# Kernel optimization log

Measured on AMD Instinct MI355X. Metric: run time of the kernel, lower is better.

Reference implementation:

```python
import jax, jax.numpy as jnp
import numpy as np

L, B, H, P = 2048, 16, 512, 256
EPS = 1e-6  # flax nnx LayerNorm default


def setup_inputs() -> dict:
    key = jax.random.key(0)
    ks = jax.random.split(key, 12)
    x = jax.random.normal(ks[0], (L, B, H), jnp.float32)
    d = jax.random.bernoulli(ks[1], 0.01, (L, B))  # sparse reset signal
    hidden_re = jnp.zeros((1, B, P), jnp.float32)
    hidden_im = jnp.zeros((1, B, P), jnp.float32)
    # S5 diagonal state matrix (stable: Re < 0)
    Lambda_re = -0.5 * jnp.exp(0.5 * jax.random.normal(ks[2], (P,), jnp.float32))
    Lambda_im = np.float32(np.pi) * jax.random.normal(ks[3], (P,), jnp.float32)
    B_re = jax.random.normal(ks[4], (P, H), jnp.float32) / np.sqrt(2.0 * H).astype(np.float32)
    B_im = jax.random.normal(ks[5], (P, H), jnp.float32) / np.sqrt(2.0 * H).astype(np.float32)
    C_re = jax.random.normal(ks[6], (H, P), jnp.float32) / np.sqrt(P).astype(np.float32)
    C_im = jax.random.normal(ks[7], (H, P), jnp.float32) / np.sqrt(P).astype(np.float32)
    D = jax.random.normal(ks[8], (H,), jnp.float32)
    log_step = jax.random.uniform(ks[9], (P,), jnp.float32,
                                  minval=np.log(1e-3).astype(np.float32),
                                  maxval=np.log(1e-1).astype(np.float32))
    ln_scale = jnp.ones((H,), jnp.float32)
    ln_bias = jnp.zeros((H,), jnp.float32)
    out2_w = jax.random.normal(ks[10], (H, H), jnp.float32) / np.sqrt(H).astype(np.float32)
    out2_b = jnp.zeros((H,), jnp.float32)
    return dict(x=x, d=d, hidden_re=hidden_re, hidden_im=hidden_im,
                Lambda_re=Lambda_re, Lambda_im=Lambda_im, B_re=B_re, B_im=B_im,
                C_re=C_re, C_im=C_im, D=D, log_step=log_step,
                ln_scale=ln_scale, ln_bias=ln_bias, out2_w=out2_w, out2_b=out2_b)


def reference(x, d, hidden_re, hidden_im, Lambda_re, Lambda_im, B_re, B_im,
              C_re, C_im, D, log_step, ln_scale, ln_bias, out2_w, out2_b):
    def ln(v):
        mu = v.mean(-1, keepdims=True)
        var = v.var(-1, keepdims=True)
        return (v - mu) * jax.lax.rsqrt(var + EPS) * ln_scale + ln_bias

    skip = x
    xn = ln(x)  # prenorm

    # --- S5 SSM (ZOH discretization), vmapped over batch == vectorized over axis 1 ---
    step = jnp.exp(log_step)  # step_rescale = 1.0
    Lam = (Lambda_re + 1j * Lambda_im).astype(jnp.complex64)          # (P,)
    Lam_bar = jnp.exp(Lam * step.astype(jnp.complex64))                # (P,)
    B_bar = ((Lam_bar - 1.0) / Lam)[:, None] * (B_re + 1j * B_im).astype(jnp.complex64)  # (P,H)
    Bu = jnp.einsum('lbh,ph->lbp', xn.astype(jnp.complex64), B_bar)    # (L,B,P)

    keep = (1.0 - d.astype(jnp.float32)).astype(jnp.complex64)         # reset zeroes the carry
    a = Lam_bar[None, None, :] * keep[:, :, None]                      # (L,B,P)
    h0 = (hidden_re + 1j * hidden_im).astype(jnp.complex64)[0]         # (B,P)
    Bu = Bu.at[0].add(a[0] * h0)                                       # fold in initial hidden

    def binop(e1, e2):
        a1, b1 = e1
        a2, b2 = e2
        return (a2 * a1, a2 * b1 + b2)

    _, xs = jax.lax.associative_scan(binop, (a, Bu), axis=0)           # (L,B,P) states
    Cmat = (C_re + 1j * C_im).astype(jnp.complex64)
    ys = 2.0 * jnp.einsum('lbp,hp->lbh', xs, Cmat).real + D * xn       # conj-sym readout + feedthrough
    new_hidden = xs[-1:]                                               # (1,B,P)

    y = ln(ys)  # gtrxl norm (shared LayerNorm)
    # half_glu2: x * sigmoid(W2 gelu(x) + b2)
    x1 = jax.nn.gelu(y)  # approximate=True matches nnx.gelu
    y = y * jax.nn.sigmoid(x1 @ out2_w + out2_b)
    out = skip + y
    return (new_hidden.real, new_hidden.imag, out)
```

## Files before the change

kernel.cpp:

```cpp
#include <hip/hip_runtime.h>

#define LL 2048
#define BB 16
#define HH 512
#define PP 256
#define MM (LL*BB)
#define NN 512
#define KK 512
#define NC 64
#define CLEN 32
#define NKT (KK/64)

typedef __bf16 bf16x8 __attribute__((ext_vector_type(8)));
typedef float  f32x4  __attribute__((ext_vector_type(4)));

__device__ __forceinline__ unsigned short f2bf(float f) {
  unsigned u = __builtin_bit_cast(unsigned, f);
  u = (u + 0x7fffu + ((u >> 16) & 1u)) >> 16;
  return (unsigned short)u;
}
__device__ __forceinline__ float bf2f(unsigned short s) {
  unsigned u = ((unsigned)s) << 16;
  return __builtin_bit_cast(float, u);
}

__global__ void detect_kernel(const unsigned int* __restrict__ dw, int* __restrict__ flag) {
  __shared__ int sInt, sFloat;
  if (threadIdx.x == 0) { sInt = 1; sFloat = 1; }
  __syncthreads();
  int allInt = 1, allFloat = 1;
  for (int i = threadIdx.x; i < 8192; i += 256) {
    unsigned v = dw[i];
    if (v > 1u) allInt = 0;
    if (v != 0u && v != 0x3f800000u) allFloat = 0;
  }
  if (!allInt) atomicAnd(&sInt, 0);
  if (!allFloat) atomicAnd(&sFloat, 0);
  __syncthreads();
  if (threadIdx.x == 0) *flag = sInt ? 0 : (sFloat ? 1 : 2);
}

__device__ __forceinline__ float keep_val(const void* d, int flag, int idx) {
  if (flag == 0) return 1.f - (float)((const int*)d)[idx];
  if (flag == 1) return 1.f - ((const float*)d)[idx];
  return 1.f - (float)((const unsigned char*)d)[idx];
}

__global__ void precompute_kernel(
    const float* __restrict__ Lre, const float* __restrict__ Lim,
    const float* __restrict__ Bre, const float* __restrict__ Bim,
    const float* __restrict__ Cre, const float* __restrict__ Cim,
    const float* __restrict__ lstep, const float* __restrict__ w2,
    unsigned short* __restrict__ W1t, unsigned short* __restrict__ W2t,
    unsigned short* __restrict__ W3t, float* __restrict__ lam_re,
    float* __restrict__ lam_im) {
  int t = blockIdx.x * 256 + threadIdx.x;
  int k = t & (KK - 1);
  int n = t >> 9;
  {
    int p = n & (PP - 1);
    float lr = Lre[p], li = Lim[p];
    float st = expf(lstep[p]);
    float er = expf(lr * st);
    float ang = li * st;
    float lbr = er * cosf(ang), lbi = er * sinf(ang);
    float den = lr * lr + li * li;
    float wr = ((lbr - 1.f) * lr + lbi * li) / den;
    float wi = (lbi * lr - (lbr - 1.f) * li) / den;
    float br = Bre[p * HH + k], bi = Bim[p * HH + k];
    float v = (n < PP) ? (wr * br - wi * bi) : (wr * bi + wi * br);
    W1t[(size_t)n * KK + k] = f2bf(v);
  }
  {
    float v = (k < PP) ? (2.f * Cre[n * PP + k]) : (-2.f * Cim[n * PP + (k - PP)]);
    W2t[(size_t)n * KK + k] = f2bf(v);
  }
  W3t[(size_t)n * KK + k] = f2bf(w2[(size_t)k * HH + n]);
  if (t < PP) {
    float lr = Lre[t], li = Lim[t];
    float st = expf(lstep[t]);
    float er = expf(lr * st);
    float ang = li * st;
    lam_re[t] = er * cosf(ang);
    lam_im[t] = er * sinf(ang);
  }
}

__global__ void ln1_kernel(const float* __restrict__ x, const float* __restrict__ sc,
                           const float* __restrict__ bs, unsigned short* __restrict__ xn) {
  int row = blockIdx.x * 4 + (threadIdx.x >> 6);
  int lane = threadIdx.x & 63;
  const float4* xr = (const float4*)(x + (size_t)row * HH) + lane * 2;
  float4 a = xr[0], b = xr[1];
  float s = (a.x + a.y) + (a.z + a.w) + (b.x + b.y) + (b.z + b.w);
  float q = a.x * a.x + a.y * a.y + a.z * a.z + a.w * a.w +
            b.x * b.x + b.y * b.y + b.z * b.z + b.w * b.w;
#pragma unroll
  for (int off = 32; off; off >>= 1) { s += __shfl_xor(s, off); q += __shfl_xor(q, off); }
  float mean = s * (1.f / HH);
  float var = fmaxf(q * (1.f / HH) - mean * mean, 0.f);
  float rstd = rsqrtf(var + 1e-6f);
  const float4* scp = (const float4*)sc + lane * 2;
  const float4* bsp = (const float4*)bs + lane * 2;
  float4 s0 = scp[0], s1 = scp[1], b0 = bsp[0], b1 = bsp[1];
  unsigned short o[8];
  o[0] = f2bf((a.x - mean) * rstd * s0.x + b0.x);
  o[1] = f2bf((a.y - mean) * rstd * s0.y + b0.y);
  o[2] = f2bf((a.z - mean) * rstd * s0.z + b0.z);
  o[3] = f2bf((a.w - mean) * rstd * s0.w + b0.w);
  o[4] = f2bf((b.x - mean) * rstd * s1.x + b1.x);
  o[5] = f2bf((b.y - mean) * rstd * s1.y + b1.y);
  o[6] = f2bf((b.z - mean) * rstd * s1.z + b1.z);
  o[7] = f2bf((b.w - mean) * rstd * s1.w + b1.w);
  uint4 pk;
  pk.x = o[0] | ((unsigned)o[1] << 16);
  pk.y = o[2] | ((unsigned)o[3] << 16);
  pk.z = o[4] | ((unsigned)o[5] << 16);
  pk.w = o[6] | ((unsigned)o[7] << 16);
  *((uint4*)(xn + (size_t)row * HH) + lane) = pk;
}

__global__ void ln2_kernel(const unsigned short* __restrict__ ys, const float* __restrict__ sc,
                           const float* __restrict__ bs, unsigned short* __restrict__ y,
                           unsigned short* __restrict__ x1) {
  int row = blockIdx.x * 4 + (threadIdx.x >> 6);
  int lane = threadIdx.x & 63;
  uint4 pin = *((const uint4*)(ys + (size_t)row * HH) + lane);
  float v[8];
  v[0] = bf2f((unsigned short)(pin.x & 0xffff)); v[1] = bf2f((unsigned short)(pin.x >> 16));
  v[2] = bf2f((unsigned short)(pin.y & 0xffff)); v[3] = bf2f((unsigned short)(pin.y >> 16));
  v[4] = bf2f((unsigned short)(pin.z & 0xffff)); v[5] = bf2f((unsigned short)(pin.z >> 16));
  v[6] = bf2f((unsigned short)(pin.w & 0xffff)); v[7] = bf2f((unsigned short)(pin.w >> 16));
  float s = 0.f, q = 0.f;
#pragma unroll
  for (int j = 0; j < 8; j++) { s += v[j]; q += v[j] * v[j]; }
#pragma unroll
  for (int off = 32; off; off >>= 1) { s += __shfl_xor(s, off); q += __shfl_xor(q, off); }
  float mean = s * (1.f / HH);
  float var = fmaxf(q * (1.f / HH) - mean * mean, 0.f);
  float rstd = rsqrtf(var + 1e-6f);
  const float4* scp = (const float4*)sc + lane * 2;
  const float4* bsp = (const float4*)bs + lane * 2;
  float4 s0 = scp[0], s1 = scp[1], b0 = bsp[0], b1 = bsp[1];
  float scv[8] = { s0.x, s0.y, s0.z, s0.w, s1.x, s1.y, s1.z, s1.w };
  float bsv[8] = { b0.x, b0.y, b0.z, b0.w, b1.x, b1.y, b1.z, b1.w };
  unsigned short oy[8], og[8];
#pragma unroll
  for (int j = 0; j < 8; j++) {
    float yv = (v[j] - mean) * rstd * scv[j] + bsv[j];
    oy[j] = f2bf(yv);
    float g = 0.5f * yv * (1.f + tanhf(0.7978845608f * (yv + 0.044715f * yv * yv * yv)));
    og[j] = f2bf(g);
  }
  uint4 py, pg;
  py.x = oy[0] | ((unsigned)oy[1] << 16); py.y = oy[2] | ((unsigned)oy[3] << 16);
  py.z = oy[4] | ((unsigned)oy[5] << 16); py.w = oy[6] | ((unsigned)oy[7] << 16);
  pg.x = og[0] | ((unsigned)og[1] << 16); pg.y = og[2] | ((unsigned)og[3] << 16);
  pg.z = og[4] | ((unsigned)og[5] << 16); pg.w = og[6] | ((unsigned)og[7] << 16);
  *((uint4*)(y  + (size_t)row * HH) + lane) = py;
  *((uint4*)(x1 + (size_t)row * HH) + lane) = pg;
}

template <int EPI>
__global__ __launch_bounds__(256, 2) void gemm_kernel(
    const unsigned short* __restrict__ A, const unsigned short* __restrict__ Wt,
    void* __restrict__ Cout, const float* __restrict__ Dvec,
    const unsigned short* __restrict__ aux16, const float* __restrict__ skip) {
  __shared__ alignas(16) unsigned short lA[2][128 * 64];
  __shared__ alignas(16) unsigned short lB[2][128 * 64];
  int tid = threadIdx.x;
  int w = tid >> 6, lane = tid & 63;
  int wgid = blockIdx.x;
  int xcd = wgid & 7, bidx = wgid >> 3;
  int m0 = (xcd * 32 + (bidx >> 2)) * 128;
  int n0 = (bidx & 3) * 128;
  int wr = w >> 1, wc = w & 1;
  f32x4 acc[4][4];
#pragma unroll
  for (int i = 0; i < 4; i++)
#pragma unroll
    for (int j = 0; j < 4; j++) acc[i][j] = (f32x4){0.f, 0.f, 0.f, 0.f};

  auto stage = [&](int buf, int kt) {
#pragma unroll
    for (int i = 0; i < 4; i++) {
      int sidx = i * 256 + tid;
      int r = sidx >> 3, c = sidx & 7;
      int cs = c ^ (r & 7);
      const unsigned short* g = A + (size_t)(m0 + r) * KK + kt * 64 + cs * 8;
      unsigned short* l = &lA[buf][(i * 256 + w * 64) * 8];
      __builtin_amdgcn_global_load_lds((const __attribute__((address_space(1))) void*)g,
                                       (__attribute__((address_space(3))) void*)l, 16, 0, 0);
    }
#pragma unroll
    for (int i = 0; i < 4; i++) {
      int sidx = i * 256 + tid;
      int r = sidx >> 3, c = sidx & 7;
      int cs = c ^ (r & 7);
      const unsigned short* g = Wt + (size_t)(n0 + r) * KK + kt * 64 + cs * 8;
      unsigned short* l = &lB[buf][(i * 256 + w * 64) * 8];
      __builtin_amdgcn_global_load_lds((const __attribute__((address_space(1))) void*)g,
                                       (__attribute__((address_space(3))) void*)l, 16, 0, 0);
    }
  };

  stage(0, 0);
  __syncthreads();
#pragma unroll
  for (int kt = 0; kt < NKT; ++kt) {
    int cur = kt & 1;
    if (kt + 1 < NKT) stage(cur ^ 1, kt + 1);
#pragma unroll
    for (int ks = 0; ks < 2; ++ks) {
      bf16x8 aF[4], bF[4];
#pragma unroll
      for (int m = 0; m < 4; m++) {
        int row = wr * 64 + m * 16 + (lane & 15);
        int s = ks * 4 + (lane >> 4);
        aF[m] = *reinterpret_cast<const bf16x8*>(&lA[cur][row * 64 + (s ^ (row & 7)) * 8]);
      }
#pragma unroll
      for (int n = 0; n < 4; n++) {
        int row = wc * 64 + n * 16 + (lane & 15);
        int s = ks * 4 + (lane >> 4);
        bF[n] = *reinterpret_cast<const bf16x8*>(&lB[cur][row * 64 + (s ^ (row & 7)) * 8]);
      }
#pragma unroll
      for (int m = 0; m < 4; m++)
#pragma unroll
        for (int n = 0; n < 4; n++)
          acc[m][n] = __builtin_amdgcn_mfma_f32_16x16x32_bf16(aF[m], bF[n], acc[m][n], 0, 0, 0);
    }
    __syncthreads();
  }
  int lr4 = (lane >> 4) * 4, lc = lane & 15;
#pragma unroll
  for (int m = 0; m < 4; m++) {
    int rowb = m0 + wr * 64 + m * 16 + lr4;
#pragma unroll
    for (int n = 0; n < 4; n++) {
      int col = n0 + wc * 64 + n * 16 + lc;
#pragma unroll
      for (int j = 0; j < 4; j++) {
        int row = rowb + j;
        size_t idxo = (size_t)row * NN + col;
        float v = acc[m][n][j];
        if (EPI == 0) {
          ((unsigned short*)Cout)[idxo] = f2bf(v);
        } else if (EPI == 1) {
          ((unsigned short*)Cout)[idxo] = f2bf(v + Dvec[col] * bf2f(aux16[idxo]));
        } else {
          float z = v + Dvec[col];
          float sg = 1.f / (1.f + expf(-z));
          ((float*)Cout)[idxo] = skip[idxo] + bf2f(aux16[idxo]) * sg;
        }
      }
    }
  }
}

__global__ void scanA_kernel(const unsigned short* __restrict__ Bu, const void* __restrict__ d,
                             const int* __restrict__ dflag, const float* __restrict__ lam_re,
                             const float* __restrict__ lam_im, float* __restrict__ Ar,
                             float* __restrict__ Ai, float* __restrict__ Sr,
                             float* __restrict__ Si) {
  int bx = blockIdx.x;
  int c = bx >> 4, b = bx & 15;
  int p = threadIdx.x;
  int fl = *dflag;
  float lr = lam_re[p], li = lam_im[p];
  float Apr = 1.f, Api = 0.f, sr = 0.f, si = 0.f;
  int l0 = c * CLEN;
  for (int j = 0; j < CLEN; j++) {
    int l = l0 + j;
    float kp = keep_val(d, fl, l * BB + b);
    float ar = lr * kp, ai = li * kp;
    size_t ro = (size_t)(l * BB + b) * NN;
    float bur = bf2f(Bu[ro + p]), bui = bf2f(Bu[ro + PP + p]);
    float nsr = ar * sr - ai * si + bur;
    float nsi = ar * si + ai * sr + bui;
    sr = nsr; si = nsi;
    float nar = ar * Apr - ai * Api;
    float nai = ar * Api + ai * Apr;
    Apr = nar; Api = nai;
  }
  int o = bx * PP + p;
  Ar[o] = Apr; Ai[o] = Api; Sr[o] = sr; Si[o] = si;
}

__global__ void scanB_kernel(const float* __restrict__ hr0, const float* __restrict__ hi0,
                             const float* __restrict__ Ar, const float* __restrict__ Ai,
                             const float* __restrict__ Sr, const float* __restrict__ Si,
                             float* __restrict__ Cr, float* __restrict__ Ci,
                             float* __restrict__ outHid) {
  int b = blockIdx.x;
  int p = threadIdx.x;
  float cr = hr0[b * PP + p], ci = hi0[b * PP + p];
  for (int c = 0; c < NC; c++) {
    int o = (c * BB + b) * PP + p;
    Cr[o] = cr; Ci[o] = ci;
    float ar = Ar[o], ai = Ai[o];
    float nr = ar * cr - ai * ci + Sr[o];
    float ni = ar * ci + ai * cr + Si[o];
    cr = nr; ci = ni;
  }
  outHid[b * PP + p] = cr;
  outHid[BB * PP + b * PP + p] = ci;
}

__global__ void scanC_kernel(const unsigned short* __restrict__ Bu, const void* __restrict__ d,
                             const int* __restrict__ dflag, const float* __restrict__ lam_re,
                             const float* __restrict__ lam_im, const float* __restrict__ Cr,
                             const float* __restrict__ Ci, unsigned short* __restrict__ xs) {
  int bx = blockIdx.x;
  int c = bx >> 4, b = bx & 15;
  int p = threadIdx.x;
  int fl = *dflag;
  float lr = lam_re[p], li = lam_im[p];
  float hr = Cr[bx * PP + p], hi = Ci[bx * PP + p];
  int l0 = c * CLEN;
  for (int j = 0; j < CLEN; j++) {
    int l = l0 + j;
    float kp = keep_val(d, fl, l * BB + b);
    float ar = lr * kp, ai = li * kp;
    size_t ro = (size_t)(l * BB + b) * NN;
    float bur = bf2f(Bu[ro + p]), bui = bf2f(Bu[ro + PP + p]);
    float nhr = ar * hr - ai * hi + bur;
    float nhi = ar * hi + ai * hr + bui;
    hr = nhr; hi = nhi;
    xs[ro + p] = f2bf(hr);
    xs[ro + PP + p] = f2bf(hi);
  }
}

extern "C" void kernel_launch(void* const* d_in, const int* in_sizes, int n_in,
                              void* d_out, int out_size, void* d_ws, size_t ws_size,
                              hipStream_t stream) {
  const float* x    = (const float*)d_in[0];
  const void*  dmask= d_in[1];
  const float* hidr = (const float*)d_in[2];
  const float* hidi = (const float*)d_in[3];
  const float* Lre  = (const float*)d_in[4];
  const float* Lim  = (const float*)d_in[5];
  const float* Bre  = (const float*)d_in[6];
  const float* Bim  = (const float*)d_in[7];
  const float* Cre  = (const float*)d_in[8];
  const float* Cim  = (const float*)d_in[9];
  const float* Dv   = (const float*)d_in[10];
  const float* lst  = (const float*)d_in[11];
  const float* lsc  = (const float*)d_in[12];
  const float* lbs  = (const float*)d_in[13];
  const float* w2   = (const float*)d_in[14];
  const float* b2   = (const float*)d_in[15];
  float* out = (float*)d_out;

  char* ws = (char*)d_ws;
  size_t off = 0;
  auto alloc = [&](size_t bytes) -> void* {
    void* p = ws + off;
    off += (bytes + 255) & ~(size_t)255;
    return p;
  };
  unsigned short* xn  = (unsigned short*)alloc((size_t)MM * KK * 2);
  unsigned short* xs  = (unsigned short*)alloc((size_t)MM * KK * 2);
  unsigned short* Bu  = (unsigned short*)alloc((size_t)MM * NN * 2);
  unsigned short* W1t = (unsigned short*)alloc((size_t)NN * KK * 2);
  unsigned short* W2t = (unsigned short*)alloc((size_t)NN * KK * 2);
  unsigned short* W3t = (unsigned short*)alloc((size_t)NN * KK * 2);
  float* lam_re = (float*)alloc(PP * 4);
  float* lam_im = (float*)alloc(PP * 4);
  float* Ar = (float*)alloc((size_t)NC * BB * PP * 4);
  float* Ai = (float*)alloc((size_t)NC * BB * PP * 4);
  float* Sr = (float*)alloc((size_t)NC * BB * PP * 4);
  float* Si = (float*)alloc((size_t)NC * BB * PP * 4);
  float* Cr = (float*)alloc((size_t)NC * BB * PP * 4);
  float* Ci = (float*)alloc((size_t)NC * BB * PP * 4);
  int* dflag = (int*)alloc(256);
  unsigned short* y   = xn;
  unsigned short* x1  = xs;
  unsigned short* ysb = Bu;

  detect_kernel<<<1, 256, 0, stream>>>((const unsigned int*)dmask, dflag);
  precompute_kernel<<<1024, 256, 0, stream>>>(Lre, Lim, Bre, Bim, Cre, Cim, lst, w2,
                                              W1t, W2t, W3t, lam_re, lam_im);
  ln1_kernel<<<MM / 4, 256, 0, stream>>>(x, lsc, lbs, xn);
  gemm_kernel<0><<<1024, 256, 0, stream>>>(xn, W1t, Bu, nullptr, nullptr, nullptr);
  scanA_kernel<<<NC * BB, 256, 0, stream>>>(Bu, dmask, dflag, lam_re, lam_im, Ar, Ai, Sr, Si);
  scanB_kernel<<<BB, 256, 0, stream>>>(hidr, hidi, Ar, Ai, Sr, Si, Cr, Ci, out);
  scanC_kernel<<<NC * BB, 256, 0, stream>>>(Bu, dmask, dflag, lam_re, lam_im, Cr, Ci, xs);
  gemm_kernel<1><<<1024, 256, 0, stream>>>(xs, W2t, ysb, Dv, xn, nullptr);
  ln2_kernel<<<MM / 4, 256, 0, stream>>>(ysb, lsc, lbs, y, x1);
  gemm_kernel<2><<<1024, 256, 0, stream>>>(x1, W3t, out + 2 * BB * PP, b2, y, x);
}
```

Baseline: 196.2 us.

## Restructure GEMM to 256x256 tiles with 8 waves and phased LDS pipeline

The GEMM kernel moves from 128x128 tiles with 4 waves to 256x256 tiles with 8 waves, using 128KB of dynamic LDS split into half-K sub-buffers. The main loop becomes eight phases per two K-tiles. Each phase interleaves a partial global->LDS stage with the MFMA block, using explicit barriers, vmcnt waits and setprio so loads overlap compute. The larger tile raises reuse per LDS byte and cuts the grid to 256 workgroups, one per CU. The cost is more register pressure (8x4 accumulators per wave) and fragile hand-written synchronisation.

Measured after the change: 199.6 us. About the same (+1.7%).

```diff
diff --git a/kernel.cpp b/kernel.cpp
--- a/kernel.cpp
+++ b/kernel.cpp
@@ -162,89 +162,114 @@
 }
 
 template <int EPI>
-__global__ __launch_bounds__(256, 2) void gemm_kernel(
+__global__ __launch_bounds__(512, 2) void gemm_kernel(
     const unsigned short* __restrict__ A, const unsigned short* __restrict__ Wt,
     void* __restrict__ Cout, const float* __restrict__ Dvec,
     const unsigned short* __restrict__ aux16, const float* __restrict__ skip) {
-  __shared__ alignas(16) unsigned short lA[2][128 * 64];
-  __shared__ alignas(16) unsigned short lB[2][128 * 64];
-  int tid = threadIdx.x;
-  int w = tid >> 6, lane = tid & 63;
-  int wgid = blockIdx.x;
-  int xcd = wgid & 7, bidx = wgid >> 3;
-  int m0 = (xcd * 32 + (bidx >> 2)) * 128;
-  int n0 = (bidx & 3) * 128;
-  int wr = w >> 1, wc = w & 1;
-  f32x4 acc[4][4];
-#pragma unroll
-  for (int i = 0; i < 4; i++)
+  extern __shared__ unsigned short smem[];
+  const int tid = threadIdx.x;
+  const int w = tid >> 6, lane = tid & 63;
+  const int wr = w >> 2, wc = w & 3;
+  const int l15 = lane & 15, g16 = lane >> 4;
+  const int wgid = blockIdx.x;
+  const int xcd = wgid & 7, bidx = wgid >> 3;
+  const int m0 = (xcd * 16 + (bidx >> 1)) * 256;
+  const int n0 = (bidx & 1) * 256;
+
+  const int rS = tid >> 2;
+  const int cgS = (tid & 3) ^ ((rS >> 1) & 3);
+
+  auto stageA = [&](int buf, int kh, int kt) {
+    const unsigned short* gp = A + (size_t)(m0 + rS) * KK + kt * 64 + kh * 32 + cgS * 8;
+    unsigned short* dp = smem + buf * 16384 + kh * 8192 + (w * 64) * 8;
+    __builtin_amdgcn_global_load_lds((const __attribute__((address_space(1))) void*)gp,
+                                     (__attribute__((address_space(3))) void*)dp, 16, 0, 0);
+    __builtin_amdgcn_global_load_lds(
+        (const __attribute__((address_space(1))) void*)(gp + (size_t)128 * KK),
+        (__attribute__((address_space(3))) void*)(dp + 512 * 8), 16, 0, 0);
+  };
+  auto stageB = [&](int buf, int kh, int kt) {
+    const unsigned short* gp = Wt + (size_t)(n0 + rS) * KK + kt * 64 + kh * 32 + cgS * 8;
+    unsigned short* dp = smem + 32768 + buf * 16384 + kh * 8192 + (w * 64) * 8;
+    __builtin_amdgcn_global_load_lds((const __attribute__((address_space(1))) void*)gp,
+                                     (__attribute__((address_space(3))) void*)dp, 16, 0, 0);
+    __builtin_amdgcn_global_load_lds(
+        (const __attribute__((address_space(1))) void*)(gp + (size_t)128 * KK),
+        (__attribute__((address_space(3))) void*)(dp + 512 * 8), 16, 0, 0);
+  };
+  auto readA = [&](int buf, int ks, int fm) -> bf16x8 {
+    int row = wr * 128 + fm * 16 + l15;
+    int ch = g16 ^ ((row >> 1) & 3);
+    return *(const bf16x8*)(smem + buf * 16384 + ks * 8192 + row * 32 + ch * 8);
+  };
+  auto readB = [&](int buf, int ks, int fn) -> bf16x8 {
+    int row = wc * 64 + fn * 16 + l15;
+    int ch = g16 ^ ((row >> 1) & 3);
+    return *(const bf16x8*)(smem + 32768 + buf * 16384 + ks * 8192 + row * 32 + ch * 8);
+  };
+
+  f32x4 acc[8][4];
+#pragma unroll
+  for (int i = 0; i < 8; i++)
 #pragma unroll
     for (int j = 0; j < 4; j++) acc[i][j] = (f32x4){0.f, 0.f, 0.f, 0.f};
-
-  auto stage = [&](int buf, int kt) {
-#pragma unroll
-    for (int i = 0; i < 4; i++) {
-      int sidx = i * 256 + tid;
-      int r = sidx >> 3, c = sidx & 7;
-      int cs = c ^ (r & 7);
-      const unsigned short* g = A + (size_t)(m0 + r) * KK + kt * 64 + cs * 8;
-      unsigned short* l = &lA[buf][(i * 256 + w * 64) * 8];
-      __builtin_amdgcn_global_load_lds((const __attribute__((address_space(1))) void*)g,
-                                       (__attribute__((address_space(3))) void*)l, 16, 0, 0);
-    }
-#pragma unroll
-    for (int i = 0; i < 4; i++) {
-      int sidx = i * 256 + tid;
-      int r = sidx >> 3, c = sidx & 7;
-      int cs = c ^ (r & 7);
-      const unsigned short* g = Wt + (size_t)(n0 + r) * KK + kt * 64 + cs * 8;
-      unsigned short* l = &lB[buf][(i * 256 + w * 64) * 8];
-      __builtin_amdgcn_global_load_lds((const __attribute__((address_space(1))) void*)g,
-                                       (__attribute__((address_space(3))) void*)l, 16, 0, 0);
-    }
-  };
-
-  stage(0, 0);
-  __syncthreads();
-#pragma unroll
-  for (int kt = 0; kt < NKT; ++kt) {
-    int cur = kt & 1;
-    if (kt + 1 < NKT) stage(cur ^ 1, kt + 1);
-#pragma unroll
-    for (int ks = 0; ks < 2; ++ks) {
-      bf16x8 aF[4], bF[4];
-#pragma unroll
-      for (int m = 0; m < 4; m++) {
-        int row = wr * 64 + m * 16 + (lane & 15);
-        int s = ks * 4 + (lane >> 4);
-        aF[m] = *reinterpret_cast<const bf16x8*>(&lA[cur][row * 64 + (s ^ (row & 7)) * 8]);
-      }
-#pragma unroll
-      for (int n = 0; n < 4; n++) {
-        int row = wc * 64 + n * 16 + (lane & 15);
-        int s = ks * 4 + (lane >> 4);
-        bF[n] = *reinterpret_cast<const bf16x8*>(&lB[cur][row * 64 + (s ^ (row & 7)) * 8]);
-      }
-#pragma unroll
-      for (int m = 0; m < 4; m++)
-#pragma unroll
-        for (int n = 0; n < 4; n++)
-          acc[m][n] = __builtin_amdgcn_mfma_f32_16x16x32_bf16(aF[m], bF[n], acc[m][n], 0, 0, 0);
-    }
-    __syncthreads();
-  }
-  int lr4 = (lane >> 4) * 4, lc = lane & 15;
-#pragma unroll
-  for (int m = 0; m < 4; m++) {
-    int rowb = m0 + wr * 64 + m * 16 + lr4;
-#pragma unroll
-    for (int n = 0; n < 4; n++) {
-      int col = n0 + wc * 64 + n * 16 + lc;
-#pragma unroll
-      for (int j = 0; j < 4; j++) {
-        int row = rowb + j;
-        size_t idxo = (size_t)row * NN + col;
-        float v = acc[m][n][j];
+  bf16x8 bF[4];
+
+#define PHASE(CB, KS, FG, STAGE_STMT, DO_VM)                                    \
+  {                                                                             \
+    bf16x8 aF[4];                                                               \
+    _Pragma("unroll") for (int fi = 0; fi < 4; fi++)                            \
+        aF[fi] = readA(CB, KS, (FG)*4 + fi);                                    \
+    if ((FG) == 0) {                                                            \
+      _Pragma("unroll") for (int fi = 0; fi < 4; fi++) bF[fi] = readB(CB, KS, fi); \
+    }                                                                           \
+    STAGE_STMT;                                                                 \
+    __builtin_amdgcn_s_barrier();                                               \
+    asm volatile("s_waitcnt lgkmcnt(0)" ::: "memory");                          \
+    __builtin_amdgcn_sched_barrier(0);                                          \
+    __builtin_amdgcn_s_setprio(1);                                              \
+    _Pragma("unroll") for (int fi = 0; fi < 4; fi++)                            \
+      _Pragma("unroll") for (int fj = 0; fj < 4; fj++)                          \
+        acc[(FG)*4 + fi][fj] = __builtin_amdgcn_mfma_f32_16x16x32_bf16(         \
+            aF[fi], bF[fj], acc[(FG)*4 + fi][fj], 0, 0, 0);                     \
+    __builtin_amdgcn_s_setprio(0);                                              \
+    if (DO_VM) asm volatile("s_waitcnt vmcnt(8)" ::: "memory");                 \
+    __builtin_amdgcn_s_barrier();                                               \
+  }
+
+  stageA(0, 0, 0); stageB(0, 0, 0);
+  stageA(0, 1, 0); stageB(0, 1, 0);
+  stageA(1, 0, 1); stageB(1, 0, 1);
+  asm volatile("s_waitcnt vmcnt(8)" ::: "memory");
+  __builtin_amdgcn_s_barrier();
+
+  for (int j = 0; j < NKT / 2; ++j) {
+    const int t1 = 2 * j + 1;
+    const int t2 = (2 * j + 2 < NKT) ? 2 * j + 2 : NKT - 1;
+    const int t3 = (2 * j + 3 < NKT) ? 2 * j + 3 : NKT - 1;
+    const bool s2 = (2 * j + 2) < NKT, s3 = (2 * j + 3) < NKT;
+    PHASE(0, 0, 0, { stageA(1, 1, t1); }, false);
+    PHASE(0, 0, 1, { stageB(1, 1, t1); }, true);
+    PHASE(0, 1, 0, { if (s2) stageA(0, 0, t2); }, false);
+    PHASE(0, 1, 1, { if (s2) stageB(0, 0, t2); }, true);
+    PHASE(1, 0, 0, { if (s2) stageA(0, 1, t2); }, false);
+    PHASE(1, 0, 1, { if (s2) stageB(0, 1, t2); }, true);
+    PHASE(1, 1, 0, { if (s3) stageA(1, 0, t3); }, false);
+    PHASE(1, 1, 1, { if (s3) stageB(1, 0, t3); }, true);
+  }
+#undef PHASE
+
+  const int lr4 = g16 * 4;
+#pragma unroll
+  for (int fm = 0; fm < 8; fm++) {
+    int rowb = m0 + wr * 128 + fm * 16 + lr4;
+#pragma unroll
+    for (int fn = 0; fn < 4; fn++) {
+      int col = n0 + wc * 64 + fn * 16 + l15;
+#pragma unroll
+      for (int jj = 0; jj < 4; jj++) {
+        size_t idxo = (size_t)(rowb + jj) * NN + col;
+        float v = acc[fm][fn][jj];
         if (EPI == 0) {
           ((unsigned short*)Cout)[idxo] = f2bf(v);
         } else if (EPI == 1) {
@@ -380,15 +405,22 @@
   unsigned short* x1  = xs;
   unsigned short* ysb = Bu;
 
+  hipFuncSetAttribute((const void*)gemm_kernel<0>,
+                      hipFuncAttributeMaxDynamicSharedMemorySize, 131072);
+  hipFuncSetAttribute((const void*)gemm_kernel<1>,
+                      hipFuncAttributeMaxDynamicSharedMemorySize, 131072);
+  hipFuncSetAttribute((const void*)gemm_kernel<2>,
+                      hipFuncAttributeMaxDynamicSharedMemorySize, 131072);
+
   detect_kernel<<<1, 256, 0, stream>>>((const unsigned int*)dmask, dflag);
   precompute_kernel<<<1024, 256, 0, stream>>>(Lre, Lim, Bre, Bim, Cre, Cim, lst, w2,
                                               W1t, W2t, W3t, lam_re, lam_im);
   ln1_kernel<<<MM / 4, 256, 0, stream>>>(x, lsc, lbs, xn);
-  gemm_kernel<0><<<1024, 256, 0, stream>>>(xn, W1t, Bu, nullptr, nullptr, nullptr);
+  gemm_kernel<0><<<256, 512, 131072, stream>>>(xn, W1t, Bu, nullptr, nullptr, nullptr);
   scanA_kernel<<<NC * BB, 256, 0, stream>>>(Bu, dmask, dflag, lam_re, lam_im, Ar, Ai, Sr, Si);
   scanB_kernel<<<BB, 256, 0, stream>>>(hidr, hidi, Ar, Ai, Sr, Si, Cr, Ci, out);
   scanC_kernel<<<NC * BB, 256, 0, stream>>>(Bu, dmask, dflag, lam_re, lam_im, Cr, Ci, xs);
-  gemm_kernel<1><<<1024, 256, 0, stream>>>(xs, W2t, ysb, Dv, xn, nullptr);
+  gemm_kernel<1><<<256, 512, 131072, stream>>>(xs, W2t, ysb, Dv, xn, nullptr);
   ln2_kernel<<<MM / 4, 256, 0, stream>>>(ysb, lsc, lbs, y, x1);
-  gemm_kernel<2><<<1024, 256, 0, stream>>>(x1, W3t, out + 2 * BB * PP, b2, y, x);
-}
+  gemm_kernel<2><<<256, 512, 131072, stream>>>(x1, W3t, out + 2 * BB * PP, b2, y, x);
+}
```

## Fuse LayerNorm2 and GELU into full-row GEMM epilogue with deeper pipelining

Applied to the files above, without the earlier changes.

Replaces the 128x128-tile GEMM with a 1024-thread kernel that computes full 128x512 output rows per block. The whole weight matrix is streamed through LDS with a three-stage B and four-stage A buffer, BK=32 and explicit vmcnt waits. Because each block owns complete rows, the second LayerNorm and the GELU can run in the GEMM epilogue through an LDS staging buffer. This removes the ln2 kernel and its round-trip of ys to memory. The cost is 128KB of dynamic LDS, lower occupancy, only 256 blocks, and hand-tuned wait counts that are fragile.

Measured after the change: 215.9 us. 1.1x slower.

```diff
diff --git a/kernel.cpp b/kernel.cpp
--- a/kernel.cpp
+++ b/kernel.cpp
@@ -9,7 +9,8 @@
 #define KK 512
 #define NC 64
 #define CLEN 32
-#define NKT (KK/64)
+#define BKF 32
+#define NKF 16
 
 typedef __bf16 bf16x8 __attribute__((ext_vector_type(8)));
 typedef float  f32x4  __attribute__((ext_vector_type(4)));
@@ -120,142 +121,180 @@
   *((uint4*)(xn + (size_t)row * HH) + lane) = pk;
 }
 
-__global__ void ln2_kernel(const unsigned short* __restrict__ ys, const float* __restrict__ sc,
-                           const float* __restrict__ bs, unsigned short* __restrict__ y,
-                           unsigned short* __restrict__ x1) {
-  int row = blockIdx.x * 4 + (threadIdx.x >> 6);
-  int lane = threadIdx.x & 63;
-  uint4 pin = *((const uint4*)(ys + (size_t)row * HH) + lane);
-  float v[8];
-  v[0] = bf2f((unsigned short)(pin.x & 0xffff)); v[1] = bf2f((unsigned short)(pin.x >> 16));
-  v[2] = bf2f((unsigned short)(pin.y & 0xffff)); v[3] = bf2f((unsigned short)(pin.y >> 16));
-  v[4] = bf2f((unsigned short)(pin.z & 0xffff)); v[5] = bf2f((unsigned short)(pin.z >> 16));
-  v[6] = bf2f((unsigned short)(pin.w & 0xffff)); v[7] = bf2f((unsigned short)(pin.w >> 16));
-  float s = 0.f, q = 0.f;
-#pragma unroll
-  for (int j = 0; j < 8; j++) { s += v[j]; q += v[j] * v[j]; }
-#pragma unroll
-  for (int off = 32; off; off >>= 1) { s += __shfl_xor(s, off); q += __shfl_xor(q, off); }
-  float mean = s * (1.f / HH);
-  float var = fmaxf(q * (1.f / HH) - mean * mean, 0.f);
-  float rstd = rsqrtf(var + 1e-6f);
-  const float4* scp = (const float4*)sc + lane * 2;
-  const float4* bsp = (const float4*)bs + lane * 2;
-  float4 s0 = scp[0], s1 = scp[1], b0 = bsp[0], b1 = bsp[1];
-  float scv[8] = { s0.x, s0.y, s0.z, s0.w, s1.x, s1.y, s1.z, s1.w };
-  float bsv[8] = { b0.x, b0.y, b0.z, b0.w, b1.x, b1.y, b1.z, b1.w };
-  unsigned short oy[8], og[8];
-#pragma unroll
-  for (int j = 0; j < 8; j++) {
-    float yv = (v[j] - mean) * rstd * scv[j] + bsv[j];
-    oy[j] = f2bf(yv);
-    float g = 0.5f * yv * (1.f + tanhf(0.7978845608f * (yv + 0.044715f * yv * yv * yv)));
-    og[j] = f2bf(g);
-  }
-  uint4 py, pg;
-  py.x = oy[0] | ((unsigned)oy[1] << 16); py.y = oy[2] | ((unsigned)oy[3] << 16);
-  py.z = oy[4] | ((unsigned)oy[5] << 16); py.w = oy[6] | ((unsigned)oy[7] << 16);
-  pg.x = og[0] | ((unsigned)og[1] << 16); pg.y = og[2] | ((unsigned)og[3] << 16);
-  pg.z = og[4] | ((unsigned)og[5] << 16); pg.w = og[6] | ((unsigned)og[7] << 16);
-  *((uint4*)(y  + (size_t)row * HH) + lane) = py;
-  *((uint4*)(x1 + (size_t)row * HH) + lane) = pg;
-}
-
 template <int EPI>
-__global__ __launch_bounds__(256, 2) void gemm_kernel(
+__global__ __launch_bounds__(1024, 4) void gemmF_kernel(
     const unsigned short* __restrict__ A, const unsigned short* __restrict__ Wt,
-    void* __restrict__ Cout, const float* __restrict__ Dvec,
-    const unsigned short* __restrict__ aux16, const float* __restrict__ skip) {
-  __shared__ alignas(16) unsigned short lA[2][128 * 64];
-  __shared__ alignas(16) unsigned short lB[2][128 * 64];
-  int tid = threadIdx.x;
-  int w = tid >> 6, lane = tid & 63;
-  int wgid = blockIdx.x;
-  int xcd = wgid & 7, bidx = wgid >> 3;
-  int m0 = (xcd * 32 + (bidx >> 2)) * 128;
-  int n0 = (bidx & 3) * 128;
-  int wr = w >> 1, wc = w & 1;
-  f32x4 acc[4][4];
-#pragma unroll
-  for (int i = 0; i < 4; i++)
-#pragma unroll
-    for (int j = 0; j < 4; j++) acc[i][j] = (f32x4){0.f, 0.f, 0.f, 0.f};
-
-  auto stage = [&](int buf, int kt) {
-#pragma unroll
-    for (int i = 0; i < 4; i++) {
-      int sidx = i * 256 + tid;
-      int r = sidx >> 3, c = sidx & 7;
-      int cs = c ^ (r & 7);
-      const unsigned short* g = A + (size_t)(m0 + r) * KK + kt * 64 + cs * 8;
-      unsigned short* l = &lA[buf][(i * 256 + w * 64) * 8];
+    void* __restrict__ out0, unsigned short* __restrict__ out1,
+    const unsigned short* __restrict__ aux16, const float* __restrict__ skip,
+    const float* __restrict__ f1, const float* __restrict__ f2,
+    const float* __restrict__ f3) {
+  extern __shared__ unsigned short smem[];
+  const int tid = threadIdx.x;
+  const int w = tid >> 6, lane = tid & 63;
+  const int wr = w >> 3, wc = w & 7;
+  const int l15 = lane & 15, g16 = lane >> 4;
+  const int m0 = blockIdx.x * 128;
+
+  const int aRow = (tid & 511) >> 2, aC = ((tid & 3) ^ (aRow & 3));
+  const int bRow = tid >> 2,        bC = ((tid & 3) ^ (bRow & 3));
+
+  auto sA = [&](int buf, int kt) {
+    if (w < 8) {
+      const unsigned short* g = A + (size_t)(m0 + aRow) * KK + kt * BKF + aC * 8;
+      unsigned short* dp = smem + buf * 4096 + (w * 64) * 8;
       __builtin_amdgcn_global_load_lds((const __attribute__((address_space(1))) void*)g,
-                                       (__attribute__((address_space(3))) void*)l, 16, 0, 0);
-    }
-#pragma unroll
-    for (int i = 0; i < 4; i++) {
-      int sidx = i * 256 + tid;
-      int r = sidx >> 3, c = sidx & 7;
-      int cs = c ^ (r & 7);
-      const unsigned short* g = Wt + (size_t)(n0 + r) * KK + kt * 64 + cs * 8;
-      unsigned short* l = &lB[buf][(i * 256 + w * 64) * 8];
-      __builtin_amdgcn_global_load_lds((const __attribute__((address_space(1))) void*)g,
-                                       (__attribute__((address_space(3))) void*)l, 16, 0, 0);
+                                       (__attribute__((address_space(3))) void*)dp, 16, 0, 0);
     }
   };
-
-  stage(0, 0);
+  auto sB = [&](int buf, int kt) {
+    const unsigned short* g = Wt + (size_t)bRow * KK + kt * BKF + bC * 8;
+    unsigned short* dp = smem + 16384 + buf * 16384 + (w * 64) * 8;
+    __builtin_amdgcn_global_load_lds((const __attribute__((address_space(1))) void*)g,
+                                     (__attribute__((address_space(3))) void*)dp, 16, 0, 0);
+    __builtin_amdgcn_global_load_lds(
+        (const __attribute__((address_space(1))) void*)(g + (size_t)256 * KK),
+        (__attribute__((address_space(3))) void*)(dp + 8192), 16, 0, 0);
+  };
+  auto rdA = [&](int buf, int fm) -> bf16x8 {
+    int row = wr * 64 + fm * 16 + l15;
+    return *(const bf16x8*)(smem + buf * 4096 + row * 32 + ((g16 ^ (row & 3)) * 8));
+  };
+  auto rdB = [&](int buf, int fn) -> bf16x8 {
+    int row = wc * 64 + fn * 16 + l15;
+    return *(const bf16x8*)(smem + 16384 + buf * 16384 + row * 32 + ((g16 ^ (row & 3)) * 8));
+  };
+
+  f32x4 acc[4][4];
+#pragma unroll
+  for (int i = 0; i < 4; i++)
+#pragma unroll
+    for (int j = 0; j < 4; j++) acc[i][j] = (f32x4){0.f, 0.f, 0.f, 0.f};
+
+  sB(0, 0); sA(0, 0); sB(1, 1); sA(1, 1); sA(2, 2);
+  if (w < 8) asm volatile("s_waitcnt vmcnt(4)" ::: "memory");
+  else       asm volatile("s_waitcnt vmcnt(2)" ::: "memory");
+  __builtin_amdgcn_s_barrier();
+
+#pragma unroll
+  for (int k = 0; k < NKF; ++k) {
+    if (k + 2 < NKF) sB((k + 2) % 3, k + 2);
+    if (k + 3 < NKF) sA((k + 3) & 3, k + 3);
+    bf16x8 aF[4];
+#pragma unroll
+    for (int fm = 0; fm < 4; fm++) aF[fm] = rdA(k & 3, fm);
+    __builtin_amdgcn_s_setprio(1);
+#pragma unroll
+    for (int fn = 0; fn < 4; fn++) {
+      bf16x8 bf = rdB(k % 3, fn);
+#pragma unroll
+      for (int fm = 0; fm < 4; fm++)
+        acc[fm][fn] = __builtin_amdgcn_mfma_f32_16x16x32_bf16(aF[fm], bf, acc[fm][fn], 0, 0, 0);
+    }
+    __builtin_amdgcn_s_setprio(0);
+    asm volatile("s_waitcnt lgkmcnt(0)" ::: "memory");
+    __builtin_amdgcn_sched_barrier(0);
+    if (k <= 12) {
+      if (w < 8) asm volatile("s_waitcnt vmcnt(4)" ::: "memory");
+      else       asm volatile("s_waitcnt vmcnt(2)" ::: "memory");
+    } else if (k == 13) {
+      if (w < 8) asm volatile("s_waitcnt vmcnt(3)" ::: "memory");
+      else       asm volatile("s_waitcnt vmcnt(2)" ::: "memory");
+    } else {
+      asm volatile("s_waitcnt vmcnt(0)" ::: "memory");
+    }
+    __builtin_amdgcn_s_barrier();
+  }
+
+  float* lf = (float*)(smem + 16384);
+  const int colb = lane * 8;
+  float cD[8], cS[8], cB[8];
+  if (EPI == 1) {
+    *(float4*)&cD[0] = *(const float4*)&f1[colb]; *(float4*)&cD[4] = *(const float4*)&f1[colb + 4];
+    *(float4*)&cS[0] = *(const float4*)&f2[colb]; *(float4*)&cS[4] = *(const float4*)&f2[colb + 4];
+    *(float4*)&cB[0] = *(const float4*)&f3[colb]; *(float4*)&cB[4] = *(const float4*)&f3[colb + 4];
+  } else if (EPI == 2) {
+    *(float4*)&cD[0] = *(const float4*)&f1[colb]; *(float4*)&cD[4] = *(const float4*)&f1[colb + 4];
+  }
   __syncthreads();
 #pragma unroll
-  for (int kt = 0; kt < NKT; ++kt) {
-    int cur = kt & 1;
-    if (kt + 1 < NKT) stage(cur ^ 1, kt + 1);
-#pragma unroll
-    for (int ks = 0; ks < 2; ++ks) {
-      bf16x8 aF[4], bF[4];
-#pragma unroll
-      for (int m = 0; m < 4; m++) {
-        int row = wr * 64 + m * 16 + (lane & 15);
-        int s = ks * 4 + (lane >> 4);
-        aF[m] = *reinterpret_cast<const bf16x8*>(&lA[cur][row * 64 + (s ^ (row & 7)) * 8]);
-      }
-#pragma unroll
-      for (int n = 0; n < 4; n++) {
-        int row = wc * 64 + n * 16 + (lane & 15);
-        int s = ks * 4 + (lane >> 4);
-        bF[n] = *reinterpret_cast<const bf16x8*>(&lB[cur][row * 64 + (s ^ (row & 7)) * 8]);
-      }
-#pragma unroll
-      for (int m = 0; m < 4; m++)
-#pragma unroll
-        for (int n = 0; n < 4; n++)
-          acc[m][n] = __builtin_amdgcn_mfma_f32_16x16x32_bf16(aF[m], bF[n], acc[m][n], 0, 0, 0);
+  for (int ch = 0; ch < 4; ++ch) {
+    if (wr == (ch >> 1)) {
+      int fmb = (ch & 1) * 2;
+#pragma unroll
+      for (int fmo = 0; fmo < 2; fmo++)
+#pragma unroll
+        for (int fn = 0; fn < 4; fn++) {
+          int col = wc * 64 + fn * 16 + l15;
+#pragma unroll
+          for (int jj = 0; jj < 4; jj++)
+            lf[(fmo * 16 + g16 * 4 + jj) * 512 + col] = acc[fmb + fmo][fn][jj];
+        }
     }
     __syncthreads();
-  }
-  int lr4 = (lane >> 4) * 4, lc = lane & 15;
-#pragma unroll
-  for (int m = 0; m < 4; m++) {
-    int rowb = m0 + wr * 64 + m * 16 + lr4;
-#pragma unroll
-    for (int n = 0; n < 4; n++) {
-      int col = n0 + wc * 64 + n * 16 + lc;
-#pragma unroll
-      for (int j = 0; j < 4; j++) {
-        int row = rowb + j;
-        size_t idxo = (size_t)row * NN + col;
-        float v = acc[m][n][j];
-        if (EPI == 0) {
-          ((unsigned short*)Cout)[idxo] = f2bf(v);
-        } else if (EPI == 1) {
-          ((unsigned short*)Cout)[idxo] = f2bf(v + Dvec[col] * bf2f(aux16[idxo]));
-        } else {
-          float z = v + Dvec[col];
-          float sg = 1.f / (1.f + expf(-z));
-          ((float*)Cout)[idxo] = skip[idxo] + bf2f(aux16[idxo]) * sg;
+#pragma unroll
+    for (int rr = 0; rr < 2; rr++) {
+      int r = w * 2 + rr;
+      int grow = m0 + ch * 32 + r;
+      float4 v0 = *(const float4*)&lf[r * 512 + colb];
+      float4 v1 = *(const float4*)&lf[r * 512 + colb + 4];
+      float v[8] = { v0.x, v0.y, v0.z, v0.w, v1.x, v1.y, v1.z, v1.w };
+      if (EPI == 0) {
+        unsigned short o[8];
+#pragma unroll
+        for (int e = 0; e < 8; e++) o[e] = f2bf(v[e]);
+        uint4 pk;
+        pk.x = o[0] | ((unsigned)o[1] << 16); pk.y = o[2] | ((unsigned)o[3] << 16);
+        pk.z = o[4] | ((unsigned)o[5] << 16); pk.w = o[6] | ((unsigned)o[7] << 16);
+        *(uint4*)(((unsigned short*)out0) + (size_t)grow * NN + colb) = pk;
+      } else if (EPI == 1) {
+        uint4 xnv = *(const uint4*)(aux16 + (size_t)grow * NN + colb);
+        unsigned xa[4] = { xnv.x, xnv.y, xnv.z, xnv.w };
+        float val[8], s = 0.f, q = 0.f;
+#pragma unroll
+        for (int e = 0; e < 8; e++) {
+          float xe = bf2f((unsigned short)((e & 1) ? (xa[e >> 1] >> 16) : (xa[e >> 1] & 0xffff)));
+          val[e] = v[e] + cD[e] * xe;
+          s += val[e]; q += val[e] * val[e];
         }
+#pragma unroll
+        for (int off = 32; off; off >>= 1) { s += __shfl_xor(s, off); q += __shfl_xor(q, off); }
+        float mean = s * (1.f / HH);
+        float var = fmaxf(q * (1.f / HH) - mean * mean, 0.f);
+        float rstd = rsqrtf(var + 1e-6f);
+        unsigned short oy[8], og[8];
+#pragma unroll
+        for (int e = 0; e < 8; e++) {
+          float yv = (val[e] - mean) * rstd * cS[e] + cB[e];
+          oy[e] = f2bf(yv);
+          float g = 0.5f * yv * (1.f + tanhf(0.7978845608f * (yv + 0.044715f * yv * yv * yv)));
+          og[e] = f2bf(g);
+        }
+        uint4 py, pg;
+        py.x = oy[0] | ((unsigned)oy[1] << 16); py.y = oy[2] | ((unsigned)oy[3] << 16);
+        py.z = oy[4] | ((unsigned)oy[5] << 16); py.w = oy[6] | ((unsigned)oy[7] << 16);
+        pg.x = og[0] | ((unsigned)og[1] << 16); pg.y = og[2] | ((unsigned)og[3] << 16);
+        pg.z = og[4] | ((unsigned)og[5] << 16); pg.w = og[6] | ((unsigned)og[7] << 16);
+        *(uint4*)(((unsigned short*)out0) + (size_t)grow * NN + colb) = py;
+        *(uint4*)(out1 + (size_t)grow * NN + colb) = pg;
+      } else {
+        uint4 yv4 = *(const uint4*)(aux16 + (size_t)grow * NN + colb);
+        unsigned ya[4] = { yv4.x, yv4.y, yv4.z, yv4.w };
+        float4 sk0 = *(const float4*)(skip + (size_t)grow * NN + colb);
+        float4 sk1 = *(const float4*)(skip + (size_t)grow * NN + colb + 4);
+        float sk[8] = { sk0.x, sk0.y, sk0.z, sk0.w, sk1.x, sk1.y, sk1.z, sk1.w };
+        float o[8];
+#pragma unroll
+        for (int e = 0; e < 8; e++) {
+          float ye = bf2f((unsigned short)((e & 1) ? (ya[e >> 1] >> 16) : (ya[e >> 1] & 0xffff)));
+          float z = v[e] + cD[e];
+          o[e] = sk[e] + ye / (1.f + expf(-z));
+        }
+        float* op = ((float*)out0) + (size_t)grow * NN + colb;
+        *(float4*)op = (float4){ o[0], o[1], o[2], o[3] };
+        *(float4*)(op + 4) = (float4){ o[4], o[5], o[6], o[7] };
       }
     }
+    __syncthreads();
   }
 }
 
@@ -364,6 +403,7 @@
   unsigned short* xn  = (unsigned short*)alloc((size_t)MM * KK * 2);
   unsigned short* xs  = (unsigned short*)alloc((size_t)MM * KK * 2);
   unsigned short* Bu  = (unsigned short*)alloc((size_t)MM * NN * 2);
+  unsigned short* x1  = (unsigned short*)alloc((size_t)MM * NN * 2);
   unsigned short* W1t = (unsigned short*)alloc((size_t)NN * KK * 2);
   unsigned short* W2t = (unsigned short*)alloc((size_t)NN * KK * 2);
   unsigned short* W3t = (unsigned short*)alloc((size_t)NN * KK * 2);
@@ -376,19 +416,25 @@
   float* Cr = (float*)alloc((size_t)NC * BB * PP * 4);
   float* Ci = (float*)alloc((size_t)NC * BB * PP * 4);
   int* dflag = (int*)alloc(256);
-  unsigned short* y   = xn;
-  unsigned short* x1  = xs;
-  unsigned short* ysb = Bu;
+  unsigned short* y = Bu;
+
+  hipFuncSetAttribute((const void*)gemmF_kernel<0>,
+                      hipFuncAttributeMaxDynamicSharedMemorySize, 131072);
+  hipFuncSetAttribute((const void*)gemmF_kernel<1>,
+                      hipFuncAttributeMaxDynamicSharedMemorySize, 131072);
+  hipFuncSetAttribute((const void*)gemmF_kernel<2>,
+                      hipFuncAttributeMaxDynamicSharedMemorySize, 131072);
 
   detect_kernel<<<1, 256, 0, stream>>>((const unsigned int*)dmask, dflag);
   precompute_kernel<<<1024, 256, 0, stream>>>(Lre, Lim, Bre, Bim, Cre, Cim, lst, w2,
                                               W1t, W2t, W3t, lam_re, lam_im);
   ln1_kernel<<<MM / 4, 256, 0, stream>>>(x, lsc, lbs, xn);
-  gemm_kernel<0><<<1024, 256, 0, stream>>>(xn, W1t, Bu, nullptr, nullptr, nullptr);
+  gemmF_kernel<0><<<256, 1024, 131072, stream>>>(xn, W1t, Bu, nullptr, nullptr, nullptr,
+                                                 nullptr, nullptr, nullptr);
   scanA_kernel<<<NC * BB, 256, 0, stream>>>(Bu, dmask, dflag, lam_re, lam_im, Ar, Ai, Sr, Si);
   scanB_kernel<<<BB, 256, 0, stream>>>(hidr, hidi, Ar, Ai, Sr, Si, Cr, Ci, out);
   scanC_kernel<<<NC * BB, 256, 0, stream>>>(Bu, dmask, dflag, lam_re, lam_im, Cr, Ci, xs);
-  gemm_kernel<1><<<1024, 256, 0, stream>>>(xs, W2t, ysb, Dv, xn, nullptr);
-  ln2_kernel<<<MM / 4, 256, 0, stream>>>(ysb, lsc, lbs, y, x1);
-  gemm_kernel<2><<<1024, 256, 0, stream>>>(x1, W3t, out + 2 * BB * PP, b2, y, x);
-}
+  gemmF_kernel<1><<<256, 1024, 131072, stream>>>(xs, W2t, y, x1, xn, nullptr, Dv, lsc, lbs);
+  gemmF_kernel<2><<<256, 1024, 131072, stream>>>(x1, W3t, out + 2 * BB * PP, nullptr, y, x,
+                                                 b2, nullptr, nullptr);
+}
```

## Load GEMM fragments directly from global and stage epilogue through LDS

Applied to the files above, without the earlier changes.

The three GEMMs no longer stage A/B tiles in double-buffered LDS. Each wave now reads its MFMA fragments straight from global memory (relying on L2 and cache reuse), and launch bounds are raised to allow more resident blocks. The epilogue is rewritten to transpose accumulators through a small padded LDS buffer, so the output, aux and skip accesses become coalesced 16-byte vector stores and loads. The cost is redundant global/L2 reads of A and B across waves and no explicit prefetch overlap.

Result: slower. 319.5 us (+62.9%).

```diff
diff --git a/kernel.cpp b/kernel.cpp
--- a/kernel.cpp
+++ b/kernel.cpp
@@ -9,7 +9,6 @@
 #define KK 512
 #define NC 64
 #define CLEN 32
-#define NKT (KK/64)
 
 typedef __bf16 bf16x8 __attribute__((ext_vector_type(8)));
 typedef float  f32x4  __attribute__((ext_vector_type(4)));
@@ -162,12 +161,11 @@
 }
 
 template <int EPI>
-__global__ __launch_bounds__(256, 2) void gemm_kernel(
+__global__ __launch_bounds__(256, 4) void gemmR_kernel(
     const unsigned short* __restrict__ A, const unsigned short* __restrict__ Wt,
     void* __restrict__ Cout, const float* __restrict__ Dvec,
     const unsigned short* __restrict__ aux16, const float* __restrict__ skip) {
-  __shared__ alignas(16) unsigned short lA[2][128 * 64];
-  __shared__ alignas(16) unsigned short lB[2][128 * 64];
+  __shared__ char lds[16896];
   int tid = threadIdx.x;
   int w = tid >> 6, lane = tid & 63;
   int wgid = blockIdx.x;
@@ -175,86 +173,134 @@
   int m0 = (xcd * 32 + (bidx >> 2)) * 128;
   int n0 = (bidx & 3) * 128;
   int wr = w >> 1, wc = w & 1;
+  const int l15 = lane & 15, g16 = lane >> 4;
+
+  const unsigned short* Ap[4];
+  const unsigned short* Bp[4];
+#pragma unroll
+  for (int i = 0; i < 4; i++) {
+    Ap[i] = A + (size_t)(m0 + wr * 64 + i * 16 + l15) * KK + g16 * 8;
+    Bp[i] = Wt + (size_t)(n0 + wc * 64 + i * 16 + l15) * KK + g16 * 8;
+  }
   f32x4 acc[4][4];
 #pragma unroll
   for (int i = 0; i < 4; i++)
 #pragma unroll
     for (int j = 0; j < 4; j++) acc[i][j] = (f32x4){0.f, 0.f, 0.f, 0.f};
 
-  auto stage = [&](int buf, int kt) {
-#pragma unroll
-    for (int i = 0; i < 4; i++) {
-      int sidx = i * 256 + tid;
-      int r = sidx >> 3, c = sidx & 7;
-      int cs = c ^ (r & 7);
-      const unsigned short* g = A + (size_t)(m0 + r) * KK + kt * 64 + cs * 8;
-      unsigned short* l = &lA[buf][(i * 256 + w * 64) * 8];
-      __builtin_amdgcn_global_load_lds((const __attribute__((address_space(1))) void*)g,
-                                       (__attribute__((address_space(3))) void*)l, 16, 0, 0);
+#pragma unroll
+  for (int kt = 0; kt < 16; ++kt) {
+    bf16x8 aF[4], bF[4];
+#pragma unroll
+    for (int i = 0; i < 4; i++) aF[i] = *(const bf16x8*)(Ap[i] + kt * 32);
+#pragma unroll
+    for (int i = 0; i < 4; i++) bF[i] = *(const bf16x8*)(Bp[i] + kt * 32);
+#pragma unroll
+    for (int m = 0; m < 4; m++)
+#pragma unroll
+      for (int n = 0; n < 4; n++)
+        acc[m][n] = __builtin_amdgcn_mfma_f32_16x16x32_bf16(aF[m], bF[n], acc[m][n], 0, 0, 0);
+  }
+  __syncthreads();
+
+  if (EPI == 0) {
+    unsigned short* lbf = (unsigned short*)lds;
+#pragma unroll
+    for (int j = 0; j < 4; j++) {
+#pragma unroll
+      for (int fn = 0; fn < 4; fn++) {
+        int col = wc * 64 + fn * 16 + l15;
+#pragma unroll
+        for (int jj = 0; jj < 4; jj++) {
+          int lrow = wr * 16 + g16 * 4 + jj;
+          lbf[lrow * 136 + col] = f2bf(acc[j][fn][jj]);
+        }
+      }
+      __syncthreads();
+#pragma unroll
+      for (int sw = 0; sw < 2; sw++) {
+        int lrow = sw * 16 + (tid >> 4);
+        int tc = tid & 15;
+        int grow = m0 + (lrow >> 4) * 64 + j * 16 + (lrow & 15);
+        int gcol = n0 + tc * 8;
+        uint4 v = *(const uint4*)&lbf[lrow * 136 + tc * 8];
+        *(uint4*)(((unsigned short*)Cout) + (size_t)grow * NN + gcol) = v;
+      }
+      __syncthreads();
     }
-#pragma unroll
-    for (int i = 0; i < 4; i++) {
-      int sidx = i * 256 + tid;
-      int r = sidx >> 3, c = sidx & 7;
-      int cs = c ^ (r & 7);
-      const unsigned short* g = Wt + (size_t)(n0 + r) * KK + kt * 64 + cs * 8;
-      unsigned short* l = &lB[buf][(i * 256 + w * 64) * 8];
-      __builtin_amdgcn_global_load_lds((const __attribute__((address_space(1))) void*)g,
-                                       (__attribute__((address_space(3))) void*)l, 16, 0, 0);
+  } else if (EPI == 1) {
+    unsigned short* lbf = (unsigned short*)lds;
+#pragma unroll
+    for (int j = 0; j < 4; j++) {
+#pragma unroll
+      for (int fn = 0; fn < 4; fn++) {
+        int col = wc * 64 + fn * 16 + l15;
+#pragma unroll
+        for (int jj = 0; jj < 4; jj++) {
+          int lrow = wr * 16 + g16 * 4 + jj;
+          lbf[lrow * 136 + col] = f2bf(acc[j][fn][jj]);
+        }
+      }
+      __syncthreads();
+#pragma unroll
+      for (int sw = 0; sw < 2; sw++) {
+        int lrow = sw * 16 + (tid >> 4);
+        int tc = tid & 15;
+        int grow = m0 + (lrow >> 4) * 64 + j * 16 + (lrow & 15);
+        int gcol = n0 + tc * 8;
+        uint4 v = *(const uint4*)&lbf[lrow * 136 + tc * 8];
+        uint4 au = *(const uint4*)(aux16 + (size_t)grow * NN + gcol);
+        float4 d0 = *(const float4*)&Dvec[gcol];
+        float4 d1 = *(const float4*)&Dvec[gcol + 4];
+        unsigned short o[8];
+        unsigned vv[4] = { v.x, v.y, v.z, v.w };
+        unsigned aa[4] = { au.x, au.y, au.z, au.w };
+        float dd[8] = { d0.x, d0.y, d0.z, d0.w, d1.x, d1.y, d1.z, d1.w };
+#pragma unroll
+        for (int e = 0; e < 8; e++) {
+          float av = bf2f((unsigned short)((e & 1) ? (vv[e >> 1] >> 16) : (vv[e >> 1] & 0xffff)));
+          float xu = bf2f((unsigned short)((e & 1) ? (aa[e >> 1] >> 16) : (aa[e >> 1] & 0xffff)));
+          o[e] = f2bf(av + dd[e] * xu);
+        }
+        uint4 pk;
+        pk.x = o[0] | ((unsigned)o[1] << 16); pk.y = o[2] | ((unsigned)o[3] << 16);
+        pk.z = o[4] | ((unsigned)o[5] << 16); pk.w = o[6] | ((unsigned)o[7] << 16);
+        *(uint4*)(((unsigned short*)Cout) + (size_t)grow * NN + gcol) = pk;
+      }
+      __syncthreads();
     }
-  };
-
-  stage(0, 0);
-  __syncthreads();
-#pragma unroll
-  for (int kt = 0; kt < NKT; ++kt) {
-    int cur = kt & 1;
-    if (kt + 1 < NKT) stage(cur ^ 1, kt + 1);
-#pragma unroll
-    for (int ks = 0; ks < 2; ++ks) {
-      bf16x8 aF[4], bF[4];
-#pragma unroll
-      for (int m = 0; m < 4; m++) {
-        int row = wr * 64 + m * 16 + (lane & 15);
-        int s = ks * 4 + (lane >> 4);
-        aF[m] = *reinterpret_cast<const bf16x8*>(&lA[cur][row * 64 + (s ^ (row & 7)) * 8]);
-      }
-#pragma unroll
-      for (int n = 0; n < 4; n++) {
-        int row = wc * 64 + n * 16 + (lane & 15);
-        int s = ks * 4 + (lane >> 4);
-        bF[n] = *reinterpret_cast<const bf16x8*>(&lB[cur][row * 64 + (s ^ (row & 7)) * 8]);
-      }
-#pragma unroll
-      for (int m = 0; m < 4; m++)
-#pragma unroll
-        for (int n = 0; n < 4; n++)
-          acc[m][n] = __builtin_amdgcn_mfma_f32_16x16x32_bf16(aF[m], bF[n], acc[m][n], 0, 0, 0);
-    }
-    __syncthreads();
-  }
-  int lr4 = (lane >> 4) * 4, lc = lane & 15;
-#pragma unroll
-  for (int m = 0; m < 4; m++) {
-    int rowb = m0 + wr * 64 + m * 16 + lr4;
-#pragma unroll
-    for (int n = 0; n < 4; n++) {
-      int col = n0 + wc * 64 + n * 16 + lc;
-#pragma unroll
-      for (int j = 0; j < 4; j++) {
-        int row = rowb + j;
-        size_t idxo = (size_t)row * NN + col;
-        float v = acc[m][n][j];
-        if (EPI == 0) {
-          ((unsigned short*)Cout)[idxo] = f2bf(v);
-        } else if (EPI == 1) {
-          ((unsigned short*)Cout)[idxo] = f2bf(v + Dvec[col] * bf2f(aux16[idxo]));
-        } else {
-          float z = v + Dvec[col];
-          float sg = 1.f / (1.f + expf(-z));
-          ((float*)Cout)[idxo] = skip[idxo] + bf2f(aux16[idxo]) * sg;
+  } else {
+    float* lf = (float*)lds;
+#pragma unroll
+    for (int j = 0; j < 4; j++) {
+#pragma unroll
+      for (int fn = 0; fn < 4; fn++) {
+        int col = wc * 64 + fn * 16 + l15;
+#pragma unroll
+        for (int jj = 0; jj < 4; jj++) {
+          int lrow = wr * 16 + g16 * 4 + jj;
+          lf[lrow * 132 + col] = acc[j][fn][jj];
         }
       }
+      __syncthreads();
+#pragma unroll
+      for (int sw = 0; sw < 4; sw++) {
+        int lrow = sw * 8 + (tid >> 5);
+        int tc = tid & 31;
+        int grow = m0 + (lrow >> 4) * 64 + j * 16 + (lrow & 15);
+        int gcol = n0 + tc * 4;
+        float4 v = *(const float4*)&lf[lrow * 132 + tc * 4];
+        float4 d = *(const float4*)&Dvec[gcol];
+        float4 sk = *(const float4*)(skip + (size_t)grow * NN + gcol);
+        ushort4 au = *(const ushort4*)(aux16 + (size_t)grow * NN + gcol);
+        float4 o;
+        o.x = sk.x + bf2f(au.x) / (1.f + expf(-(v.x + d.x)));
+        o.y = sk.y + bf2f(au.y) / (1.f + expf(-(v.y + d.y)));
+        o.z = sk.z + bf2f(au.z) / (1.f + expf(-(v.z + d.z)));
+        o.w = sk.w + bf2f(au.w) / (1.f + expf(-(v.w + d.w)));
+        *(float4*)(((float*)Cout) + (size_t)grow * NN + gcol) = o;
+      }
+      __syncthreads();
     }
   }
 }
@@ -384,11 +430,11 @@
   precompute_kernel<<<1024, 256, 0, stream>>>(Lre, Lim, Bre, Bim, Cre, Cim, lst, w2,
                                               W1t, W2t, W3t, lam_re, lam_im);
   ln1_kernel<<<MM / 4, 256, 0, stream>>>(x, lsc, lbs, xn);
-  gemm_kernel<0><<<1024, 256, 0, stream>>>(xn, W1t, Bu, nullptr, nullptr, nullptr);
+  gemmR_kernel<0><<<1024, 256, 0, stream>>>(xn, W1t, Bu, nullptr, nullptr, nullptr);
   scanA_kernel<<<NC * BB, 256, 0, stream>>>(Bu, dmask, dflag, lam_re, lam_im, Ar, Ai, Sr, Si);
   scanB_kernel<<<BB, 256, 0, stream>>>(hidr, hidi, Ar, Ai, Sr, Si, Cr, Ci, out);
   scanC_kernel<<<NC * BB, 256, 0, stream>>>(Bu, dmask, dflag, lam_re, lam_im, Cr, Ci, xs);
-  gemm_kernel<1><<<1024, 256, 0, stream>>>(xs, W2t, ysb, Dv, xn, nullptr);
+  gemmR_kernel<1><<<1024, 256, 0, stream>>>(xs, W2t, ysb, Dv, xn, nullptr);
   ln2_kernel<<<MM / 4, 256, 0, stream>>>(ysb, lsc, lbs, y, x1);
-  gemm_kernel<2><<<1024, 256, 0, stream>>>(x1, W3t, out + 2 * BB * PP, b2, y, x);
-}
+  gemmR_kernel<2><<<1024, 256, 0, stream>>>(x1, W3t, out + 2 * BB * PP, b2, y, x);
+}
```
